# Performance work log

Hardware: AMD Instinct MI355X
Metric: run time of the kernel (lower is better)

The kernel has to match this reference:

```python
import jax, jax.numpy as jnp
import numpy as np

B, S, HID = 2, 2048, 768
NH, HD = 12, 64
WINDOW_HALF = 64  # local_attention // 2
ROPE_THETA = 10000.0  # local_rope_theta (layer_id=1 -> local layer)


def setup_inputs() -> dict:
    key = jax.random.key(0)
    k1, k2, k3 = jax.random.split(key, 3)
    hidden_states = jax.random.normal(k1, (B, S, HID), dtype=jnp.float32)
    Wqkv_w = jax.random.normal(k2, (3 * HID, HID), dtype=jnp.float32) * (1.0 / np.sqrt(HID))
    Wo_w = jax.random.normal(k3, (HID, HID), dtype=jnp.float32) * (1.0 / np.sqrt(HID))
    # additive sliding-window mask: 0 inside +/-WINDOW_HALF band, finfo.min outside
    idx = jnp.arange(S)
    band = jnp.abs(idx[:, None] - idx[None, :]) <= WINDOW_HALF
    neg = jnp.finfo(jnp.float32).min
    sliding_window_mask = jnp.where(band, 0.0, neg)[None, None, :, :].astype(jnp.float32)
    position_ids = jnp.tile(jnp.arange(S, dtype=jnp.int64)[None, :], (B, 1))
    return {
        "hidden_states": hidden_states,
        "Wqkv_w": Wqkv_w,
        "Wo_w": Wo_w,
        "sliding_window_mask": sliding_window_mask,
        "position_ids": position_ids,
    }


def _rotate_half(x):
    x1, x2 = jnp.split(x, 2, axis=-1)
    return jnp.concatenate((-x2, x1), axis=-1)


def _rope_cos_sin(position_ids):
    # inv_freq: [HD//2]
    inv_freq = 1.0 / (ROPE_THETA ** (jnp.arange(0, HD, 2, dtype=jnp.float32) / HD))
    freqs = position_ids.astype(jnp.float32)[:, :, None] * inv_freq[None, None, :]  # [B,S,HD//2]
    emb = jnp.concatenate((freqs, freqs), axis=-1)  # [B,S,HD]
    return jnp.cos(emb), jnp.sin(emb)


def reference(hidden_states, Wqkv_w, Wo_w, sliding_window_mask, position_ids):
    bs, s, _ = hidden_states.shape
    qkv = hidden_states @ Wqkv_w.T  # [B,S,3*HID]
    qkv = qkv.reshape(bs, s, 3, NH, HD)
    # transpose(3,1).unbind(2) -> q,k,v each [B,NH,S,HD]
    qkv = jnp.transpose(qkv, (0, 3, 2, 1, 4))
    q, k, v = qkv[:, :, 0], qkv[:, :, 1], qkv[:, :, 2]
    cos, sin = _rope_cos_sin(position_ids)  # [B,S,HD]
    cos = cos[:, None, :, :].astype(hidden_states.dtype)
    sin = sin[:, None, :, :].astype(hidden_states.dtype)
    q = q * cos + _rotate_half(q) * sin
    k = k * cos + _rotate_half(k) * sin
    scale = 1.0 / np.sqrt(HD)
    scores = jnp.einsum("bhqd,bhkd->bhqk", q, k) * scale + sliding_window_mask
    probs = jax.nn.softmax(scores, axis=-1)
    attn = jnp.einsum("bhqk,bhkd->bhqd", probs, v)  # [B,NH,S,HD]
    attn = jnp.transpose(attn, (0, 2, 1, 3)).reshape(bs, s, NH * HD)
    return attn @ Wo_w.T
```

## Files before the change

kernel.cpp:

```cpp
#include <hip/hip_runtime.h>
#include <hip/hip_bf16.h>
#include <cstdint>

typedef __bf16 bf16_t;
typedef __bf16 bf16x8 __attribute__((ext_vector_type(8)));
typedef float f32x4 __attribute__((ext_vector_type(4)));

#define B_    2
#define S_    2048
#define HID_  768
#define NH_   12
#define HD_   64
#define KDIM_ 768

#define N_HID_  3145728
#define N_WQKV_ 1769472
#define N_WO_   589824

__device__ __forceinline__ void glds16(const bf16_t* g, const bf16_t* lds) {
  __builtin_amdgcn_global_load_lds((const __attribute__((address_space(1))) void*)g,
                                   (__attribute__((address_space(3))) void*)lds,
                                   16, 0, 0);
}

__global__ __launch_bounds__(256) void cvt3_kernel(
    const float* __restrict__ a, const float* __restrict__ b, const float* __restrict__ c,
    bf16_t* __restrict__ da, bf16_t* __restrict__ db, bf16_t* __restrict__ dc)
{
  size_t i = ((size_t)blockIdx.x * 256 + threadIdx.x) * 8;
  const float* s; bf16_t* d; size_t off;
  if (i < N_HID_)                { s = a; d = da; off = i; }
  else if (i < N_HID_ + N_WQKV_) { s = b; d = db; off = i - N_HID_; }
  else                           { s = c; d = dc; off = i - (N_HID_ + N_WQKV_); }
  float4 v0 = *(const float4*)(s + off);
  float4 v1 = *(const float4*)(s + off + 4);
  bf16x8 o;
  o[0] = (bf16_t)v0.x; o[1] = (bf16_t)v0.y; o[2] = (bf16_t)v0.z; o[3] = (bf16_t)v0.w;
  o[4] = (bf16_t)v1.x; o[5] = (bf16_t)v1.y; o[6] = (bf16_t)v1.z; o[7] = (bf16_t)v1.w;
  *(bf16x8*)(d + off) = o;
}

template<int MODE, int BM, int BN>
__launch_bounds__(256, 4)
__global__ void gemm_kernel(const bf16_t* __restrict__ A,
                            const bf16_t* __restrict__ Bw,
                            bf16_t* __restrict__ Qo,
                            bf16_t* __restrict__ Ko,
                            bf16_t* __restrict__ Vo,
                            float* __restrict__ outf)
{
  constexpr int MACC = BM / 32;
  constexpr int NWF  = BN / 32;
  __shared__ bf16_t As[BM * 64];
  __shared__ bf16_t Bs[BN * 64];

  const int tid  = threadIdx.x;
  const int w    = tid >> 6;
  const int lane = tid & 63;
  const int wm   = w >> 1, wn = w & 1;
  const int m0   = blockIdx.y * BM;
  const int n0   = blockIdx.x * BN;
  const int lr   = lane >> 3;
  const int sub  = lane & 7;

  f32x4 acc[MACC][NWF];
#pragma unroll
  for (int i = 0; i < MACC; i++)
#pragma unroll
    for (int j = 0; j < NWF; j++) acc[i][j] = f32x4{0.f, 0.f, 0.f, 0.f};

  for (int k0 = 0; k0 < KDIM_; k0 += 64) {
#pragma unroll
    for (int q = 0; q < MACC; ++q) {
      const int row = q * 32 + w * 8 + lr;
      const int c16 = sub ^ (row & 7);
      glds16(A + (size_t)(m0 + row) * KDIM_ + k0 + c16 * 8, &As[(q * 32 + w * 8) * 64]);
    }
#pragma unroll
    for (int q = 0; q < NWF; ++q) {
      const int row = q * 32 + w * 8 + lr;
      const int c16 = sub ^ (row & 7);
      glds16(Bw + (size_t)(n0 + row) * KDIM_ + k0 + c16 * 8, &Bs[(q * 32 + w * 8) * 64]);
    }
    __syncthreads();

#pragma unroll
    for (int kk = 0; kk < 2; ++kk) {
      const int su = kk * 4 + (lane >> 4);
      bf16x8 af[MACC], bfr[NWF];
#pragma unroll
      for (int m = 0; m < MACC; m++) {
        const int row = wm * (BM / 2) + m * 16 + (lane & 15);
        af[m] = *(const bf16x8*)&As[row * 64 + (su ^ (row & 7)) * 8];
      }
#pragma unroll
      for (int n = 0; n < NWF; n++) {
        const int row = wn * (BN / 2) + n * 16 + (lane & 15);
        bfr[n] = *(const bf16x8*)&Bs[row * 64 + (su ^ (row & 7)) * 8];
      }
#pragma unroll
      for (int m = 0; m < MACC; m++)
#pragma unroll
        for (int n = 0; n < NWF; n++)
          acc[m][n] = __builtin_amdgcn_mfma_f32_16x16x32_bf16(af[m], bfr[n], acc[m][n], 0, 0, 0);
    }
    __syncthreads();
  }

  const int c = lane & 15;
  if constexpr (MODE == 1) {
#pragma unroll
    for (int m = 0; m < MACC; m++)
#pragma unroll
      for (int r = 0; r < 4; r++) {
        const int row = m0 + wm * (BM / 2) + m * 16 + (lane >> 4) * 4 + r;
#pragma unroll
        for (int nf = 0; nf < NWF; nf++)
          outf[(size_t)row * HID_ + n0 + wn * (BN / 2) + nf * 16 + c] = acc[m][nf][r];
      }
  } else {
    const int slot  = blockIdx.x * 2 + wn;
    const int which = slot / NH_;
    const int h     = slot % NH_;
    bf16_t* dst = (which == 0) ? Qo : (which == 1 ? Ko : Vo);
    const float NL = -13.287712379549449f / 32.0f;
    const float invf0 = exp2f((float)c * NL);
    const float invf1 = exp2f((float)(16 + c) * NL);
#pragma unroll
    for (int m = 0; m < MACC; m++)
#pragma unroll
      for (int r = 0; r < 4; r++) {
        const int row = m0 + wm * (BM / 2) + m * 16 + (lane >> 4) * 4 + r;
        const int b = row >> 11, s = row & 2047;
        const size_t base = ((size_t)(b * NH_ + h) * S_ + s) * HD_;
        if (which == 2) {
#pragma unroll
          for (int nf = 0; nf < 4; nf++)
            dst[base + nf * 16 + c] = (bf16_t)acc[m][nf][r];
        } else {
#pragma unroll
          for (int nf = 0; nf < 2; nf++) {
            float sn, cs;
            __sincosf((float)s * (nf ? invf1 : invf0), &sn, &cs);
            const float x1 = acc[m][nf][r], x2 = acc[m][nf + 2][r];
            dst[base + nf * 16 + c]      = (bf16_t)(x1 * cs - x2 * sn);
            dst[base + 32 + nf * 16 + c] = (bf16_t)(x2 * cs + x1 * sn);
          }
        }
      }
  }
}

__launch_bounds__(128, 4)
__global__ void attn_kernel(const bf16_t* __restrict__ Qw,
                            const bf16_t* __restrict__ Kw,
                            const bf16_t* __restrict__ Vw,
                            bf16_t* __restrict__ Ob)
{
  __shared__ bf16_t Vt[64 * 192];
  __shared__ bf16_t Pl[2][16 * 192];

  const int tid  = threadIdx.x;
  const int w    = tid >> 6;
  const int lane = tid & 63;
  const int bxq  = blockIdx.x;
  const int h    = blockIdx.y, b = blockIdx.z;
  const size_t base = (size_t)(b * NH_ + h) * S_ * HD_;
  const int kb = bxq * 32 - 64;

  const int i0 = bxq * 32 + w * 16;
  bf16x8 qf[2];
#pragma unroll
  for (int kk = 0; kk < 2; kk++)
    qf[kk] = *(const bf16x8*)(Qw + base + (size_t)(i0 + (lane & 15)) * HD_ + kk * 32 + (lane >> 4) * 8);

  {
#pragma unroll
    for (int it = 0; it < 10; ++it) {
      const int bk = it * 16 + (tid >> 3);
      const int d0 = (tid & 7) * 8;
      int j = kb + bk; j = j < 0 ? 0 : (j > S_ - 1 ? S_ - 1 : j);
      bf16x8 v = *(const bf16x8*)(Vw + base + (size_t)j * HD_ + d0);
      const int gsw = (((bk >> 3) ^ (tid & 7)) << 3) + (bk & 7);
#pragma unroll
      for (int e = 0; e < 8; e++) Vt[(d0 + e) * 192 + gsw] = v[e];
    }
    const bf16x8 z8 = {};
#pragma unroll
    for (int zz = 0; zz < 2; ++zz) {
      const int idx = zz * 128 + tid;
      const int d = idx >> 2, g = 20 + (idx & 3);
      *(bf16x8*)&Vt[d * 192 + ((g ^ (d >> 3)) << 3)] = z8;
    }
  }
  __syncthreads();

  f32x4 sc[9];
#pragma unroll
  for (int t = 0; t < 9; t++) sc[t] = f32x4{0.f, 0.f, 0.f, 0.f};
#pragma unroll
  for (int kk = 0; kk < 2; kk++) {
    const int su = kk * 4 + (lane >> 4);
#pragma unroll
    for (int t = 0; t < 9; t++) {
      const int bk = w * 16 + t * 16 + (lane & 15);
      int j = kb + bk; j = j < 0 ? 0 : (j > S_ - 1 ? S_ - 1 : j);
      bf16x8 kf = *(const bf16x8*)(Kw + base + (size_t)j * HD_ + su * 8);
      sc[t] = __builtin_amdgcn_mfma_f32_16x16x32_bf16(qf[kk], kf, sc[t], 0, 0, 0);
    }
  }

  const int c  = lane & 15;
  const int qh = lane >> 4;
  float lrow[4];
#pragma unroll
  for (int r = 0; r < 4; r++) {
    const int i = i0 + qh * 4 + r;
    float mx = -1e30f;
#pragma unroll
    for (int t = 0; t < 9; t++) {
      const int j = kb + w * 16 + t * 16 + c;
      const int dd = j - i;
      const bool valid = (dd >= -64) && (dd <= 64) && (j >= 0) && (j < S_);
      const float v = valid ? sc[t][r] * 0.125f : -1e30f;
      sc[t][r] = v;
      mx = fmaxf(mx, v);
    }
    mx = fmaxf(mx, __shfl_xor(mx, 1, 16));
    mx = fmaxf(mx, __shfl_xor(mx, 2, 16));
    mx = fmaxf(mx, __shfl_xor(mx, 4, 16));
    mx = fmaxf(mx, __shfl_xor(mx, 8, 16));
    float sum = 0.f;
#pragma unroll
    for (int t = 0; t < 9; t++) {
      const float p = __expf(sc[t][r] - mx);
      sc[t][r] = p;
      sum += p;
    }
    sum += __shfl_xor(sum, 1, 16);
    sum += __shfl_xor(sum, 2, 16);
    sum += __shfl_xor(sum, 4, 16);
    sum += __shfl_xor(sum, 8, 16);
    lrow[r] = sum;
  }

#pragma unroll
  for (int t = 0; t < 9; t++)
#pragma unroll
    for (int r = 0; r < 4; r++) {
      const int row = qh * 4 + r;
      const int col = t * 16 + c;
      Pl[w][row * 192 + (((col >> 3) ^ (row & 7)) << 3) + (col & 7)] = (bf16_t)sc[t][r];
    }
  {
    const bf16x8 z8 = {};
    const int row = lane & 15, g = 18 + ((lane >> 4) & 1);
    *(bf16x8*)&Pl[w][row * 192 + ((g ^ (row & 7)) << 3)] = z8;
  }
  asm volatile("s_waitcnt lgkmcnt(0)" ::: "memory");
  __builtin_amdgcn_sched_barrier(0);

  f32x4 ao[4];
#pragma unroll
  for (int nf = 0; nf < 4; nf++) ao[nf] = f32x4{0.f, 0.f, 0.f, 0.f};
#pragma unroll
  for (int kc = 0; kc < 5; kc++) {
    const int prow = lane & 15;
    const int Lp = kc * 32 + (lane >> 4) * 8;
    bf16x8 pf = *(const bf16x8*)&Pl[w][prow * 192 + (((Lp >> 3) ^ (prow & 7)) << 3)];
#pragma unroll
    for (int nf = 0; nf < 4; nf++) {
      const int d = nf * 16 + (lane & 15);
      const int L = w * 16 + Lp;
      bf16x8 vf = *(const bf16x8*)&Vt[d * 192 + (((L >> 3) ^ (d >> 3)) << 3)];
      ao[nf] = __builtin_amdgcn_mfma_f32_16x16x32_bf16(pf, vf, ao[nf], 0, 0, 0);
    }
  }

#pragma unroll
  for (int r = 0; r < 4; r++) {
    const float inv = 1.0f / lrow[r];
    const int srow = i0 + qh * 4 + r;
    const size_t orow = ((size_t)(b * S_ + srow)) * HID_ + h * HD_;
#pragma unroll
    for (int nf = 0; nf < 4; nf++)
      Ob[orow + nf * 16 + c] = (bf16_t)(ao[nf][r] * inv);
  }
}

extern "C" void kernel_launch(void* const* d_in, const int* in_sizes, int n_in,
                              void* d_out, int out_size, void* d_ws, size_t ws_size,
                              hipStream_t stream) {
  const float* hidden_f = (const float*)d_in[0];
  const float* wqkv_f   = (const float*)d_in[1];
  const float* wo_f     = (const float*)d_in[2];

  bf16_t* ws = (bf16_t*)d_ws;
  size_t off = 0;
  bf16_t* Hb    = ws + off; off += N_HID_;
  bf16_t* Wqkvb = ws + off; off += N_WQKV_;
  bf16_t* Wob   = ws + off; off += N_WO_;
  const size_t E = (size_t)B_ * NH_ * S_ * HD_;
  bf16_t* Q    = ws + off; off += E;
  bf16_t* K    = ws + off; off += E;
  bf16_t* V    = ws + off; off += E;
  bf16_t* ABUF = ws + off; off += E;
  float*  out  = (float*)d_out;

  cvt3_kernel<<<dim3((N_HID_ + N_WQKV_ + N_WO_) / (256 * 8)), dim3(256), 0, stream>>>(
      hidden_f, wqkv_f, wo_f, Hb, Wqkvb, Wob);
  gemm_kernel<0, 64, 128><<<dim3(18, 64), dim3(256), 0, stream>>>(Hb, Wqkvb, Q, K, V, nullptr);
  attn_kernel<<<dim3(64, 12, 2), dim3(128), 0, stream>>>(Q, K, V, ABUF);
  gemm_kernel<1, 64, 64><<<dim3(12, 64), dim3(256), 0, stream>>>(ABUF, Wob, nullptr, nullptr, nullptr, out);
}
```

Measured before the change: 68.93 us.

## Replace LDS-staged GEMM with direct register loads and double buffering

The GEMM kernel no longer stages tiles through shared memory with global_load_lds and barriers. Each lane now loads its MFMA fragments straight from global memory into registers, with a two-deep register prefetch across the fully unrolled K loop. BM grows to 128 for both GEMMs and occupancy bounds drop to 2 to fit the extra registers. This removes the LDS traffic and syncthreads, but each wave now reads its operands separately with less coalesced access and no shared reuse across waves.

New measurement: 134.0 us. 1.94x slower.

```diff
diff --git a/kernel.cpp b/kernel.cpp
--- a/kernel.cpp
+++ b/kernel.cpp
@@ -16,12 +16,6 @@
 #define N_HID_  3145728
 #define N_WQKV_ 1769472
 #define N_WO_   589824
-
-__device__ __forceinline__ void glds16(const bf16_t* g, const bf16_t* lds) {
-  __builtin_amdgcn_global_load_lds((const __attribute__((address_space(1))) void*)g,
-                                   (__attribute__((address_space(3))) void*)lds,
-                                   16, 0, 0);
-}
 
 __global__ __launch_bounds__(256) void cvt3_kernel(
     const float* __restrict__ a, const float* __restrict__ b, const float* __restrict__ c,
@@ -41,7 +35,7 @@
 }
 
 template<int MODE, int BM, int BN>
-__launch_bounds__(256, 4)
+__launch_bounds__(256, 2)
 __global__ void gemm_kernel(const bf16_t* __restrict__ A,
                             const bf16_t* __restrict__ Bw,
                             bf16_t* __restrict__ Qo,
@@ -51,8 +45,7 @@
 {
   constexpr int MACC = BM / 32;
   constexpr int NWF  = BN / 32;
-  __shared__ bf16_t As[BM * 64];
-  __shared__ bf16_t Bs[BN * 64];
+  constexpr int NU   = KDIM_ / 32;
 
   const int tid  = threadIdx.x;
   const int w    = tid >> 6;
@@ -60,8 +53,6 @@
   const int wm   = w >> 1, wn = w & 1;
   const int m0   = blockIdx.y * BM;
   const int n0   = blockIdx.x * BN;
-  const int lr   = lane >> 3;
-  const int sub  = lane & 7;
 
   f32x4 acc[MACC][NWF];
 #pragma unroll
@@ -69,42 +60,37 @@
 #pragma unroll
     for (int j = 0; j < NWF; j++) acc[i][j] = f32x4{0.f, 0.f, 0.f, 0.f};
 
-  for (int k0 = 0; k0 < KDIM_; k0 += 64) {
-#pragma unroll
-    for (int q = 0; q < MACC; ++q) {
-      const int row = q * 32 + w * 8 + lr;
-      const int c16 = sub ^ (row & 7);
-      glds16(A + (size_t)(m0 + row) * KDIM_ + k0 + c16 * 8, &As[(q * 32 + w * 8) * 64]);
-    }
-#pragma unroll
-    for (int q = 0; q < NWF; ++q) {
-      const int row = q * 32 + w * 8 + lr;
-      const int c16 = sub ^ (row & 7);
-      glds16(Bw + (size_t)(n0 + row) * KDIM_ + k0 + c16 * 8, &Bs[(q * 32 + w * 8) * 64]);
-    }
-    __syncthreads();
-
-#pragma unroll
-    for (int kk = 0; kk < 2; ++kk) {
-      const int su = kk * 4 + (lane >> 4);
-      bf16x8 af[MACC], bfr[NWF];
-#pragma unroll
-      for (int m = 0; m < MACC; m++) {
-        const int row = wm * (BM / 2) + m * 16 + (lane & 15);
-        af[m] = *(const bf16x8*)&As[row * 64 + (su ^ (row & 7)) * 8];
-      }
-#pragma unroll
-      for (int n = 0; n < NWF; n++) {
-        const int row = wn * (BN / 2) + n * 16 + (lane & 15);
-        bfr[n] = *(const bf16x8*)&Bs[row * 64 + (su ^ (row & 7)) * 8];
-      }
-#pragma unroll
-      for (int m = 0; m < MACC; m++)
-#pragma unroll
-        for (int n = 0; n < NWF; n++)
-          acc[m][n] = __builtin_amdgcn_mfma_f32_16x16x32_bf16(af[m], bfr[n], acc[m][n], 0, 0, 0);
-    }
-    __syncthreads();
+  const int klane = (lane >> 4) * 8;
+  const bf16_t* aPtr[MACC];
+  const bf16_t* bPtr[NWF];
+#pragma unroll
+  for (int m = 0; m < MACC; m++)
+    aPtr[m] = A + (size_t)(m0 + wm * (BM / 2) + m * 16 + (lane & 15)) * KDIM_ + klane;
+#pragma unroll
+  for (int n = 0; n < NWF; n++)
+    bPtr[n] = Bw + (size_t)(n0 + wn * (BN / 2) + n * 16 + (lane & 15)) * KDIM_ + klane;
+
+  bf16x8 af[2][MACC], bfr[2][NWF];
+#pragma unroll
+  for (int m = 0; m < MACC; m++) af[0][m] = *(const bf16x8*)(aPtr[m]);
+#pragma unroll
+  for (int n = 0; n < NWF; n++) bfr[0][n] = *(const bf16x8*)(bPtr[n]);
+
+#pragma unroll
+  for (int u = 0; u < NU; ++u) {
+    const int cb = u & 1, nb = cb ^ 1;
+    if (u < NU - 1) {
+      const int ko = (u + 1) * 32;
+#pragma unroll
+      for (int m = 0; m < MACC; m++) af[nb][m] = *(const bf16x8*)(aPtr[m] + ko);
+#pragma unroll
+      for (int n = 0; n < NWF; n++) bfr[nb][n] = *(const bf16x8*)(bPtr[n] + ko);
+    }
+#pragma unroll
+    for (int m = 0; m < MACC; m++)
+#pragma unroll
+      for (int n = 0; n < NWF; n++)
+        acc[m][n] = __builtin_amdgcn_mfma_f32_16x16x32_bf16(af[cb][m], bfr[cb][n], acc[m][n], 0, 0, 0);
   }
 
   const int c = lane & 15;
@@ -309,7 +295,7 @@
 
   cvt3_kernel<<<dim3((N_HID_ + N_WQKV_ + N_WO_) / (256 * 8)), dim3(256), 0, stream>>>(
       hidden_f, wqkv_f, wo_f, Hb, Wqkvb, Wob);
-  gemm_kernel<0, 64, 128><<<dim3(18, 64), dim3(256), 0, stream>>>(Hb, Wqkvb, Q, K, V, nullptr);
+  gemm_kernel<0, 128, 128><<<dim3(18, 32), dim3(256), 0, stream>>>(Hb, Wqkvb, Q, K, V, nullptr);
   attn_kernel<<<dim3(64, 12, 2), dim3(128), 0, stream>>>(Q, K, V, ABUF);
-  gemm_kernel<1, 64, 64><<<dim3(12, 64), dim3(256), 0, stream>>>(ABUF, Wob, nullptr, nullptr, nullptr, out);
+  gemm_kernel<1, 128, 64><<<dim3(12, 32), dim3(256), 0, stream>>>(ABUF, Wob, nullptr, nullptr, nullptr, out);
 }
```

## Generalize GEMM tiling, enlarge QKV tile, remap blocks for XCD locality, raise MFMA priority

Applied to the files above, without the earlier changes.

Parameterizes the GEMM kernel over block tile, wave grid and thread count. The QKV projection moves to a 128x128 tile with 8 waves (512 threads) to get more operand reuse per LDS load. Both GEMMs now use a 1D grid whose block index is remapped so that consecutive blocks on each XCD cover a contiguous chunk of tiles, aiming at better L2 locality. It also raises wave priority around the MFMA loop and skips the final barrier. The larger tile halves the QKV grid, which may cost occupancy and load balance.

Measured after the change: 63.68 us. 7.6% less time.

```diff
diff --git a/kernel.cpp b/kernel.cpp
--- a/kernel.cpp
+++ b/kernel.cpp
@@ -40,8 +40,8 @@
   *(bf16x8*)(d + off) = o;
 }
 
-template<int MODE, int BM, int BN>
-__launch_bounds__(256, 4)
+template<int MODE, int BM, int BN, int WM, int WN, int NTHR, int MINW, int NTX, int CHUNK>
+__launch_bounds__(NTHR, MINW)
 __global__ void gemm_kernel(const bf16_t* __restrict__ A,
                             const bf16_t* __restrict__ Bw,
                             bf16_t* __restrict__ Qo,
@@ -49,19 +49,22 @@
                             bf16_t* __restrict__ Vo,
                             float* __restrict__ outf)
 {
-  constexpr int MACC = BM / 32;
-  constexpr int NWF  = BN / 32;
+  constexpr int W    = WM * WN;
+  constexpr int MACC = BM / WM / 16;
+  constexpr int NWF  = BN / WN / 16;
   __shared__ bf16_t As[BM * 64];
   __shared__ bf16_t Bs[BN * 64];
 
   const int tid  = threadIdx.x;
   const int w    = tid >> 6;
   const int lane = tid & 63;
-  const int wm   = w >> 1, wn = w & 1;
-  const int m0   = blockIdx.y * BM;
-  const int n0   = blockIdx.x * BN;
-  const int lr   = lane >> 3;
-  const int sub  = lane & 7;
+  const int wm   = w / WN, wn = w % WN;
+  const int wk = (blockIdx.x & 7) * CHUNK + (blockIdx.x >> 3);
+  const int tx = wk % NTX, ty = wk / NTX;
+  const int m0 = ty * BM;
+  const int n0 = tx * BN;
+  const int lr  = lane >> 3;
+  const int sub = lane & 7;
 
   f32x4 acc[MACC][NWF];
 #pragma unroll
@@ -71,16 +74,14 @@
 
   for (int k0 = 0; k0 < KDIM_; k0 += 64) {
 #pragma unroll
-    for (int q = 0; q < MACC; ++q) {
-      const int row = q * 32 + w * 8 + lr;
-      const int c16 = sub ^ (row & 7);
-      glds16(A + (size_t)(m0 + row) * KDIM_ + k0 + c16 * 8, &As[(q * 32 + w * 8) * 64]);
-    }
-#pragma unroll
-    for (int q = 0; q < NWF; ++q) {
-      const int row = q * 32 + w * 8 + lr;
-      const int c16 = sub ^ (row & 7);
-      glds16(Bw + (size_t)(n0 + row) * KDIM_ + k0 + c16 * 8, &Bs[(q * 32 + w * 8) * 64]);
+    for (int q = 0; q < BM / 8 / W; ++q) {
+      const int rb = (q * W + w) * 8, row = rb + lr;
+      glds16(A + (size_t)(m0 + row) * KDIM_ + k0 + (sub ^ (row & 7)) * 8, &As[rb * 64]);
+    }
+#pragma unroll
+    for (int q = 0; q < BN / 8 / W; ++q) {
+      const int rb = (q * W + w) * 8, row = rb + lr;
+      glds16(Bw + (size_t)(n0 + row) * KDIM_ + k0 + (sub ^ (row & 7)) * 8, &Bs[rb * 64]);
     }
     __syncthreads();
 
@@ -90,21 +91,23 @@
       bf16x8 af[MACC], bfr[NWF];
 #pragma unroll
       for (int m = 0; m < MACC; m++) {
-        const int row = wm * (BM / 2) + m * 16 + (lane & 15);
+        const int row = wm * (BM / WM) + m * 16 + (lane & 15);
         af[m] = *(const bf16x8*)&As[row * 64 + (su ^ (row & 7)) * 8];
       }
 #pragma unroll
       for (int n = 0; n < NWF; n++) {
-        const int row = wn * (BN / 2) + n * 16 + (lane & 15);
+        const int row = wn * (BN / WN) + n * 16 + (lane & 15);
         bfr[n] = *(const bf16x8*)&Bs[row * 64 + (su ^ (row & 7)) * 8];
       }
+      __builtin_amdgcn_s_setprio(1);
 #pragma unroll
       for (int m = 0; m < MACC; m++)
 #pragma unroll
         for (int n = 0; n < NWF; n++)
           acc[m][n] = __builtin_amdgcn_mfma_f32_16x16x32_bf16(af[m], bfr[n], acc[m][n], 0, 0, 0);
-    }
-    __syncthreads();
+      __builtin_amdgcn_s_setprio(0);
+    }
+    if (k0 < KDIM_ - 64) __syncthreads();
   }
 
   const int c = lane & 15;
@@ -113,13 +116,13 @@
     for (int m = 0; m < MACC; m++)
 #pragma unroll
       for (int r = 0; r < 4; r++) {
-        const int row = m0 + wm * (BM / 2) + m * 16 + (lane >> 4) * 4 + r;
+        const int row = m0 + wm * (BM / WM) + m * 16 + (lane >> 4) * 4 + r;
 #pragma unroll
         for (int nf = 0; nf < NWF; nf++)
-          outf[(size_t)row * HID_ + n0 + wn * (BN / 2) + nf * 16 + c] = acc[m][nf][r];
+          outf[(size_t)row * HID_ + n0 + wn * (BN / WN) + nf * 16 + c] = acc[m][nf][r];
       }
   } else {
-    const int slot  = blockIdx.x * 2 + wn;
+    const int slot  = tx * (BN / 64) + wn;
     const int which = slot / NH_;
     const int h     = slot % NH_;
     bf16_t* dst = (which == 0) ? Qo : (which == 1 ? Ko : Vo);
@@ -130,7 +133,7 @@
     for (int m = 0; m < MACC; m++)
 #pragma unroll
       for (int r = 0; r < 4; r++) {
-        const int row = m0 + wm * (BM / 2) + m * 16 + (lane >> 4) * 4 + r;
+        const int row = m0 + wm * (BM / WM) + m * 16 + (lane >> 4) * 4 + r;
         const int b = row >> 11, s = row & 2047;
         const size_t base = ((size_t)(b * NH_ + h) * S_ + s) * HD_;
         if (which == 2) {
@@ -309,7 +312,9 @@
 
   cvt3_kernel<<<dim3((N_HID_ + N_WQKV_ + N_WO_) / (256 * 8)), dim3(256), 0, stream>>>(
       hidden_f, wqkv_f, wo_f, Hb, Wqkvb, Wob);
-  gemm_kernel<0, 64, 128><<<dim3(18, 64), dim3(256), 0, stream>>>(Hb, Wqkvb, Q, K, V, nullptr);
+  gemm_kernel<0, 128, 128, 4, 2, 512, 4, 18, 72><<<dim3(576), dim3(512), 0, stream>>>(
+      Hb, Wqkvb, Q, K, V, nullptr);
   attn_kernel<<<dim3(64, 12, 2), dim3(128), 0, stream>>>(Q, K, V, ABUF);
-  gemm_kernel<1, 64, 64><<<dim3(12, 64), dim3(256), 0, stream>>>(ABUF, Wob, nullptr, nullptr, nullptr, out);
-}
+  gemm_kernel<1, 64, 64, 2, 2, 256, 4, 12, 96><<<dim3(768), dim3(256), 0, stream>>>(
+      ABUF, Wob, nullptr, nullptr, nullptr, out);
+}
```
